# Kernel tuning notes

Measured on AMD Instinct MI355X. Metric: run time of the kernel, lower is better.

Reference implementation:

```python
import jax, jax.numpy as jnp
import numpy as np
import math

B, C, HLAT, WLON = 1, 256, 46, 90
HEADS = 8
KC = 256   # k_channels (defaults to in_channels)
OC = 256   # out_channels (defaults to in_channels)


def _cc_weights(n):
    # Clenshaw-Curtis quadrature weights on n nodes x_k = cos(k*pi/(n-1)) over [-1, 1]
    # (torch-harmonics 'equiangular' grid quadrature); weights sum to 2.
    N = n - 1
    k = np.arange(n)
    j = np.arange(1, N // 2 + 1)
    b = np.where(2 * j == N, 1.0, 2.0)
    s = (b / (4.0 * j**2 - 1.0))[None, :] * np.cos(2.0 * np.pi * np.outer(k, j) / N)
    w = (1.0 - s.sum(axis=1)) * (2.0 / N)
    w[0] *= 0.5
    w[-1] *= 0.5
    return w


def _log_quad_weights(nlat, nlon):
    wgl = _cc_weights(nlat).astype(np.float32)            # [nlat]
    qw = 2.0 * np.pi * wgl / nlon                          # [nlat]
    qw = np.tile(qw.reshape(-1, 1), (1, nlon)).flatten()   # [nlat*nlon]
    return np.log(qw).reshape(1, 1, -1)                    # (1, 1, N)


def setup_inputs() -> dict:
    key = jax.random.key(0)
    ks = jax.random.split(key, 6)
    scale_qkv = math.sqrt(3.0 / C)
    scale_proj = math.sqrt(3.0 / OC)
    uni = lambda k, shp, s: s * (2.0 * jax.random.uniform(k, shp, dtype=jnp.float32) - 1.0)
    return {
        "query": jax.random.normal(ks[0], (B, C, HLAT, WLON), dtype=jnp.float32),
        "q_w": uni(ks[1], (KC, C), scale_qkv),
        "q_b": jnp.zeros((KC,), dtype=jnp.float32),
        "k_w": uni(ks[2], (KC, C), scale_qkv),
        "k_b": jnp.zeros((KC,), dtype=jnp.float32),
        "v_w": uni(ks[3], (OC, C), scale_qkv),
        "v_b": jnp.zeros((OC,), dtype=jnp.float32),
        "p_w": uni(ks[4], (OC, OC), scale_proj),
        "p_b": jnp.zeros((OC,), dtype=jnp.float32),
        "log_qw": jnp.asarray(_log_quad_weights(HLAT, WLON)),
    }


def _conv1x1(x, w, b):
    # 1x1 conv == per-pixel channel GEMM
    return jnp.einsum("bchw,kc->bkhw", x, w) + b[None, :, None, None]


def _to_seq(x, heads):
    # [B, heads*d, H, W] -> [B, heads, H*W, d]
    b, c, h, w = x.shape
    d = c // heads
    return x.reshape(b, heads, d, h, w).transpose(0, 1, 3, 4, 2).reshape(b, heads, h * w, d)


def reference(query, q_w, q_b, k_w, k_b, v_w, v_b, p_w, p_b, log_qw):
    # key = value = query (self-attention path of the module)
    q = _conv1x1(query, q_w, q_b)
    k = _conv1x1(query, k_w, k_b)
    v = _conv1x1(query, v_w, v_b)

    qs = _to_seq(q, HEADS)   # [B, h, N, dk]
    ks = _to_seq(k, HEADS)   # [B, h, M, dk]
    vs = _to_seq(v, HEADS)   # [B, h, M, dv]

    dk = KC // HEADS
    scale = 1.0 / math.sqrt(dk)  # SDPA default scale
    # scores with additive log-quadrature-weight bias over keys
    scores = jnp.einsum("bhnd,bhmd->bhnm", qs, ks) * scale + log_qw[:, :, None, :]
    attn = jax.nn.softmax(scores, axis=-1)
    out = jnp.einsum("bhnm,bhmd->bhnd", attn, vs)  # [B, h, N, dv]

    bb, hh, nn, dv = out.shape
    out = out.transpose(0, 1, 3, 2).reshape(bb, hh * dv, HLAT, WLON)
    out = _conv1x1(out, p_w, p_b)
    return out
```

## Files before the change

kernel.cpp:

```cpp
#include <hip/hip_runtime.h>

#define N_SEQ 4140
#define NP    4160
#define C_IN  256
#define HEADS 8
#define NT32  130
#define HN    (HEADS * N_SEQ)
#define LOG2E 1.4426950408889634f
#define SCALE2 (0.17677669529663687f * LOG2E)

typedef _Float16 f16x8 __attribute__((ext_vector_type(8)));
typedef _Float16 f16x2 __attribute__((ext_vector_type(2)));
typedef float    f32x16 __attribute__((ext_vector_type(16)));

__device__ inline unsigned short f16b(float x) {
    union { _Float16 h; unsigned short s; } c;
    c.h = (_Float16)x;
    return c.s;
}
__device__ inline f16x2 pkrtz(float a, float b) {
    auto r = __builtin_amdgcn_cvt_pkrtz(a, b);
    union { decltype(r) i; f16x2 o; } c;
    c.i = r;
    return c.o;
}
__device__ inline void permswap(unsigned &a, unsigned &b) {
    asm volatile("v_permlane32_swap_b32 %0, %1" : "+v"(a), "+v"(b));
}

__global__ __launch_bounds__(256) void prep_kernel(
    const float* __restrict__ x, const float* __restrict__ log_qw,
    const float* __restrict__ q_w, const float* __restrict__ k_w,
    const float* __restrict__ v_w, const float* __restrict__ p_w,
    unsigned short* __restrict__ xt, float* __restrict__ lw2,
    unsigned short* __restrict__ wf, unsigned short* __restrict__ pwf)
{
    if (blockIdx.x < NT32) {
        __shared__ unsigned short tile[32][33];
        const int tx = threadIdx.x & 31, ty = threadIdx.x >> 5;
        const int n0 = blockIdx.x * 32, c0 = blockIdx.y * 32;
#pragma unroll
        for (int i = 0; i < 4; ++i) {
            const int c = c0 + ty * 4 + i;
            const int n = n0 + tx;
            const float v = (n < N_SEQ) ? x[(size_t)c * N_SEQ + n] : 0.f;
            tile[tx][ty * 4 + i] = f16b(v);
        }
        __syncthreads();
#pragma unroll
        for (int i = 0; i < 4; ++i) {
            const int nl = ty * 4 + i;
            xt[(size_t)(n0 + nl) * C_IN + c0 + tx] = tile[nl][tx];
        }
    } else {
        const int bid = (blockIdx.x - NT32) * 8 + blockIdx.y;
        for (int i = bid * 256 + threadIdx.x; i < 262144 + NP; i += 24 * 256) {
            if (i < 65536)        wf[i] = f16b(q_w[i] * SCALE2);
            else if (i < 131072)  wf[i] = f16b(k_w[i - 65536]);
            else if (i < 196608)  wf[i] = f16b(v_w[i - 131072]);
            else if (i < 262144)  pwf[i - 196608] = f16b(p_w[i - 196608]);
            else {
                const int j = i - 262144;
                lw2[j] = (j < N_SEQ) ? log_qw[j] * LOG2E : -1e30f;
            }
        }
    }
}

__global__ __launch_bounds__(64) void qkv_mfma(
    const unsigned short* __restrict__ xt, const unsigned short* __restrict__ wf,
    const float* __restrict__ q_b, const float* __restrict__ k_b,
    const float* __restrict__ v_b,
    unsigned short* __restrict__ qo, unsigned short* __restrict__ ko,
    unsigned short* __restrict__ vo)
{
    const int lane = threadIdx.x;
    const int col = lane & 31, hi = lane >> 5;
    const int bid = blockIdx.x;
    const int ot = bid / NT32, nt = bid % NT32;
    const int n0 = nt * 32;

    if (ot < 16) {
        const unsigned short* arow = xt + (size_t)(n0 + col) * C_IN + hi * 8;
        const unsigned short* brow = wf + (size_t)(ot * 32 + col) * C_IN + hi * 8;
        const float bias = (ot < 8) ? q_b[ot * 32 + col] * SCALE2
                                    : k_b[(ot - 8) * 32 + col];
        f32x16 acc0, acc1;
#pragma unroll
        for (int r = 0; r < 16; ++r) { acc0[r] = bias; acc1[r] = 0.f; }
#pragma unroll
        for (int t = 0; t < 8; ++t) {
            const f16x8 af0 = *(const f16x8*)(const void*)(arow + t * 16);
            const f16x8 bf0 = *(const f16x8*)(const void*)(brow + t * 16);
            const f16x8 af1 = *(const f16x8*)(const void*)(arow + (t + 8) * 16);
            const f16x8 bf1 = *(const f16x8*)(const void*)(brow + (t + 8) * 16);
            acc0 = __builtin_amdgcn_mfma_f32_32x32x16_f16(af0, bf0, acc0, 0, 0, 0);
            acc1 = __builtin_amdgcn_mfma_f32_32x32x16_f16(af1, bf1, acc1, 0, 0, 0);
        }
        unsigned short* dst = (ot < 8) ? qo : ko;
        const int h = ot & 7;
#pragma unroll
        for (int r = 0; r < 16; ++r) {
            const int rl = (r & 3) + 8 * (r >> 2) + 4 * hi;
            dst[(size_t)(h * NP + n0 + rl) * 32 + col] = f16b(acc0[r] + acc1[r]);
        }
    } else {
        const int h = ot - 16;
        const unsigned short* arow = wf + (size_t)(512 + h * 32 + col) * C_IN + hi * 8;
        const unsigned short* brow = xt + (size_t)(n0 + col) * C_IN + hi * 8;
        const float* vb4 = v_b + h * 32 + 4 * hi;
        const float4 c0 = *(const float4*)(vb4);
        const float4 c1 = *(const float4*)(vb4 + 8);
        const float4 c2 = *(const float4*)(vb4 + 16);
        const float4 c3 = *(const float4*)(vb4 + 24);
        f32x16 acc0, acc1;
        acc0[0]=c0.x; acc0[1]=c0.y; acc0[2]=c0.z; acc0[3]=c0.w;
        acc0[4]=c1.x; acc0[5]=c1.y; acc0[6]=c1.z; acc0[7]=c1.w;
        acc0[8]=c2.x; acc0[9]=c2.y; acc0[10]=c2.z; acc0[11]=c2.w;
        acc0[12]=c3.x; acc0[13]=c3.y; acc0[14]=c3.z; acc0[15]=c3.w;
#pragma unroll
        for (int r = 0; r < 16; ++r) acc1[r] = 0.f;
#pragma unroll
        for (int t = 0; t < 8; ++t) {
            const f16x8 af0 = *(const f16x8*)(const void*)(arow + t * 16);
            const f16x8 bf0 = *(const f16x8*)(const void*)(brow + t * 16);
            const f16x8 af1 = *(const f16x8*)(const void*)(arow + (t + 8) * 16);
            const f16x8 bf1 = *(const f16x8*)(const void*)(brow + (t + 8) * 16);
            acc0 = __builtin_amdgcn_mfma_f32_32x32x16_f16(af0, bf0, acc0, 0, 0, 0);
            acc1 = __builtin_amdgcn_mfma_f32_32x32x16_f16(af1, bf1, acc1, 0, 0, 0);
        }
#pragma unroll
        for (int r = 0; r < 16; ++r) {
            const int d = (r & 3) + 8 * (r >> 2) + 4 * hi;
            vo[((size_t)(h * NT32 + nt) * 32 + d) * 32 + col] = f16b(acc0[r] + acc1[r]);
        }
    }
}

__global__ __launch_bounds__(64) void attn_mfma_kernel(
    const unsigned short* __restrict__ qb, const unsigned short* __restrict__ kb,
    const unsigned short* __restrict__ vb, const float* __restrict__ lw2,
    float* __restrict__ pm, float* __restrict__ pl, float* __restrict__ pacc,
    int tiles_per_z)
{
    const int lane = threadIdx.x;
    const int col = lane & 31;
    const int hi = lane >> 5;
    const int job = blockIdx.x;
    const int h = job / 65;
    const int pt = job % 65;
    const int z = blockIdx.y;

    const int qrowA = pt * 64 + col;
    const int qrowB = qrowA + 32;
    const unsigned short* qpA = qb + ((size_t)(h * NP + qrowA)) * 32 + hi * 8;
    const unsigned short* qpB = qb + ((size_t)(h * NP + qrowB)) * 32 + hi * 8;
    const f16x8 qfA0 = *(const f16x8*)(const void*)(qpA);
    const f16x8 qfA1 = *(const f16x8*)(const void*)(qpA + 16);
    const f16x8 qfB0 = *(const f16x8*)(const void*)(qpB);
    const f16x8 qfB1 = *(const f16x8*)(const void*)(qpB + 16);

    f32x16 oA, oB;
#pragma unroll
    for (int r = 0; r < 16; ++r) { oA[r] = 0.f; oB[r] = 0.f; }
    float mA = -1e30f, lsA = 0.f;
    float mB = -1e30f, lsB = 0.f;
    const f16x2 one2 = { (_Float16)1.f, (_Float16)1.f };

    const int t0 = z * tiles_per_z;
    const int t1 = min(NT32, t0 + tiles_per_z);
    const unsigned short* kbase = kb + (size_t)h * NP * 32;
    const unsigned short* vbase = vb + (size_t)h * NT32 * 1024;

    for (int t = t0; t < t1; ++t) {
        const int k0 = t * 32;
        const unsigned short* kp = kbase + (size_t)(k0 + col) * 32 + hi * 8;
        const f16x8 ka0 = *(const f16x8*)(const void*)(kp);
        const f16x8 ka1 = *(const f16x8*)(const void*)(kp + 16);
        const unsigned short* vp = vbase + (size_t)t * 1024 + col * 32 + hi * 8;
        const f16x8 va0 = *(const f16x8*)(const void*)(vp);
        const f16x8 va1 = *(const f16x8*)(const void*)(vp + 16);

        const float* lw4 = lw2 + k0 + 4 * hi;
        const float4 w0 = *(const float4*)(lw4);
        const float4 w1 = *(const float4*)(lw4 + 8);
        const float4 w2 = *(const float4*)(lw4 + 16);
        const float4 w3 = *(const float4*)(lw4 + 24);
        f32x16 sA;
        sA[0]=w0.x; sA[1]=w0.y; sA[2]=w0.z; sA[3]=w0.w;
        sA[4]=w1.x; sA[5]=w1.y; sA[6]=w1.z; sA[7]=w1.w;
        sA[8]=w2.x; sA[9]=w2.y; sA[10]=w2.z; sA[11]=w2.w;
        sA[12]=w3.x; sA[13]=w3.y; sA[14]=w3.z; sA[15]=w3.w;
        f32x16 sB = sA;

        sA = __builtin_amdgcn_mfma_f32_32x32x16_f16(ka0, qfA0, sA, 0, 0, 0);
        sB = __builtin_amdgcn_mfma_f32_32x32x16_f16(ka0, qfB0, sB, 0, 0, 0);
        sA = __builtin_amdgcn_mfma_f32_32x32x16_f16(ka1, qfA1, sA, 0, 0, 0);
        sB = __builtin_amdgcn_mfma_f32_32x32x16_f16(ka1, qfB1, sB, 0, 0, 0);

        const float a0m = fmaxf(fmaxf(sA[0], sA[1]), sA[2]);
        const float a1m = fmaxf(fmaxf(sA[3], sA[4]), sA[5]);
        const float a2m = fmaxf(fmaxf(sA[6], sA[7]), sA[8]);
        const float a3m = fmaxf(fmaxf(sA[9], sA[10]), sA[11]);
        const float a4m = fmaxf(fmaxf(sA[12], sA[13]), sA[14]);
        const float cmaxA = fmaxf(fmaxf(fmaxf(a0m, a1m), a2m),
                                  fmaxf(fmaxf(a3m, a4m), sA[15]));
        const float b0m = fmaxf(fmaxf(sB[0], sB[1]), sB[2]);
        const float b1m = fmaxf(fmaxf(sB[3], sB[4]), sB[5]);
        const float b2m = fmaxf(fmaxf(sB[6], sB[7]), sB[8]);
        const float b3m = fmaxf(fmaxf(sB[9], sB[10]), sB[11]);
        const float b4m = fmaxf(fmaxf(sB[12], sB[13]), sB[14]);
        const float cmaxB = fmaxf(fmaxf(fmaxf(b0m, b1m), b2m),
                                  fmaxf(fmaxf(b3m, b4m), sB[15]));

        if (!__all(cmaxA - mA <= 8.0f)) {
            float cw = fmaxf(cmaxA, __shfl_xor(cmaxA, 32));
            const float mnew = fmaxf(mA, cw);
            const float esc = __builtin_amdgcn_exp2f(mA - mnew);
            lsA *= esc;
#pragma unroll
            for (int r = 0; r < 16; ++r) oA[r] *= esc;
            mA = mnew;
        }
        if (!__all(cmaxB - mB <= 8.0f)) {
            float cw = fmaxf(cmaxB, __shfl_xor(cmaxB, 32));
            const float mnew = fmaxf(mB, cw);
            const float esc = __builtin_amdgcn_exp2f(mB - mnew);
            lsB *= esc;
#pragma unroll
            for (int r = 0; r < 16; ++r) oB[r] *= esc;
            mB = mnew;
        }

        float pA[16], pB[16];
#pragma unroll
        for (int r = 0; r < 16; ++r) {
            pA[r] = __builtin_amdgcn_exp2f(sA[r] - mA);
            pB[r] = __builtin_amdgcn_exp2f(sB[r] - mB);
        }

        union PK { f16x2 h[4]; unsigned u[4]; f16x8 v; };
        {
            PK k0p, k1p;
            k0p.h[0] = pkrtz(pA[0], pA[1]);
            k0p.h[1] = pkrtz(pA[2], pA[3]);
            k0p.h[2] = pkrtz(pA[4], pA[5]);
            k0p.h[3] = pkrtz(pA[6], pA[7]);
            k1p.h[0] = pkrtz(pA[8], pA[9]);
            k1p.h[1] = pkrtz(pA[10], pA[11]);
            k1p.h[2] = pkrtz(pA[12], pA[13]);
            k1p.h[3] = pkrtz(pA[14], pA[15]);
            float sa = __builtin_amdgcn_fdot2(k0p.h[0], one2, 0.f, false);
            float sb = __builtin_amdgcn_fdot2(k0p.h[1], one2, 0.f, false);
            sa = __builtin_amdgcn_fdot2(k0p.h[2], one2, sa, false);
            sb = __builtin_amdgcn_fdot2(k0p.h[3], one2, sb, false);
            sa = __builtin_amdgcn_fdot2(k1p.h[0], one2, sa, false);
            sb = __builtin_amdgcn_fdot2(k1p.h[1], one2, sb, false);
            sa = __builtin_amdgcn_fdot2(k1p.h[2], one2, sa, false);
            sb = __builtin_amdgcn_fdot2(k1p.h[3], one2, sb, false);
            lsA += sa + sb;
            permswap(k0p.u[0], k0p.u[2]);
            permswap(k0p.u[1], k0p.u[3]);
            oA = __builtin_amdgcn_mfma_f32_32x32x16_f16(va0, k0p.v, oA, 0, 0, 0);
            permswap(k1p.u[0], k1p.u[2]);
            permswap(k1p.u[1], k1p.u[3]);
            oA = __builtin_amdgcn_mfma_f32_32x32x16_f16(va1, k1p.v, oA, 0, 0, 0);
        }
        {
            PK k0p, k1p;
            k0p.h[0] = pkrtz(pB[0], pB[1]);
            k0p.h[1] = pkrtz(pB[2], pB[3]);
            k0p.h[2] = pkrtz(pB[4], pB[5]);
            k0p.h[3] = pkrtz(pB[6], pB[7]);
            k1p.h[0] = pkrtz(pB[8], pB[9]);
            k1p.h[1] = pkrtz(pB[10], pB[11]);
            k1p.h[2] = pkrtz(pB[12], pB[13]);
            k1p.h[3] = pkrtz(pB[14], pB[15]);
            float sa = __builtin_amdgcn_fdot2(k0p.h[0], one2, 0.f, false);
            float sb = __builtin_amdgcn_fdot2(k0p.h[1], one2, 0.f, false);
            sa = __builtin_amdgcn_fdot2(k0p.h[2], one2, sa, false);
            sb = __builtin_amdgcn_fdot2(k0p.h[3], one2, sb, false);
            sa = __builtin_amdgcn_fdot2(k1p.h[0], one2, sa, false);
            sb = __builtin_amdgcn_fdot2(k1p.h[1], one2, sb, false);
            sa = __builtin_amdgcn_fdot2(k1p.h[2], one2, sa, false);
            sb = __builtin_amdgcn_fdot2(k1p.h[3], one2, sb, false);
            lsB += sa + sb;
            permswap(k0p.u[0], k0p.u[2]);
            permswap(k0p.u[1], k0p.u[3]);
            oB = __builtin_amdgcn_mfma_f32_32x32x16_f16(va0, k0p.v, oB, 0, 0, 0);
            permswap(k1p.u[0], k1p.u[2]);
            permswap(k1p.u[1], k1p.u[3]);
            oB = __builtin_amdgcn_mfma_f32_32x32x16_f16(va1, k1p.v, oB, 0, 0, 0);
        }
    }

    lsA += __shfl_xor(lsA, 32);
    lsB += __shfl_xor(lsB, 32);

    if (qrowA < N_SEQ) {
        const size_t qi = (size_t)h * N_SEQ + qrowA;
        if (hi == 0) {
            pm[(size_t)z * HN + qi] = mA;
            pl[(size_t)z * HN + qi] = lsA;
        }
        float* pa = pacc + ((size_t)z * HN + qi) * 32;
#pragma unroll
        for (int r = 0; r < 16; ++r)
            pa[(r & 3) + 8 * (r >> 2) + 4 * hi] = oA[r];
    }
    if (qrowB < N_SEQ) {
        const size_t qi = (size_t)h * N_SEQ + qrowB;
        if (hi == 0) {
            pm[(size_t)z * HN + qi] = mB;
            pl[(size_t)z * HN + qi] = lsB;
        }
        float* pa = pacc + ((size_t)z * HN + qi) * 32;
#pragma unroll
        for (int r = 0; r < 16; ++r)
            pa[(r & 3) + 8 * (r >> 2) + 4 * hi] = oB[r];
    }
}

__global__ __launch_bounds__(256) void merge_kernel(
    const float* __restrict__ pm, const float* __restrict__ pl,
    const float* __restrict__ pacc, unsigned short* __restrict__ at_t, int nz)
{
    const int gid = blockIdx.x * 256 + threadIdx.x;
    if (gid >= HN * 4) return;
    const int idx = gid >> 2;
    const int sub = gid & 3;
    const int h = idx / N_SEQ;
    const int n = idx - h * N_SEQ;

    float mg = pm[idx];
    for (int zz = 1; zz < nz; ++zz) mg = fmaxf(mg, pm[(size_t)zz * HN + idx]);

    float lg = 0.f;
    float acc[8];
#pragma unroll
    for (int d = 0; d < 8; ++d) acc[d] = 0.f;
    for (int zz = 0; zz < nz; ++zz) {
        const float e = exp2f(pm[(size_t)zz * HN + idx] - mg);
        lg += pl[(size_t)zz * HN + idx] * e;
        const float* pa = pacc + ((size_t)zz * HN + idx) * 32 + sub * 8;
#pragma unroll
        for (int d = 0; d < 8; ++d) acc[d] = fmaf(pa[d], e, acc[d]);
    }
    const float inv = 1.0f / lg;
    union { unsigned short s[8]; uint4 u; } ph;
#pragma unroll
    for (int d = 0; d < 8; ++d) ph.s[d] = f16b(acc[d] * inv);
    *(uint4*)(at_t + (size_t)n * C_IN + h * 32 + sub * 8) = ph.u;
}

__global__ __launch_bounds__(64) void proj_mfma(
    const unsigned short* __restrict__ at_t, const unsigned short* __restrict__ pwf,
    const float* __restrict__ p_b, float* __restrict__ out)
{
    const int lane = threadIdx.x;
    const int col = lane & 31, hi = lane >> 5;
    const int tile = blockIdx.x;
    const int ot = tile / NT32, nt = tile % NT32;
    const int n0 = nt * 32;

    const unsigned short* arow = pwf + (size_t)(ot * 32 + col) * C_IN + hi * 8;
    const unsigned short* brow = at_t + (size_t)(n0 + col) * C_IN + hi * 8;

    const float* pb4 = p_b + ot * 32 + 4 * hi;
    const float4 c0 = *(const float4*)(pb4);
    const float4 c1 = *(const float4*)(pb4 + 8);
    const float4 c2 = *(const float4*)(pb4 + 16);
    const float4 c3 = *(const float4*)(pb4 + 24);
    f32x16 acca, accb;
    acca[0]=c0.x; acca[1]=c0.y; acca[2]=c0.z; acca[3]=c0.w;
    acca[4]=c1.x; acca[5]=c1.y; acca[6]=c1.z; acca[7]=c1.w;
    acca[8]=c2.x; acca[9]=c2.y; acca[10]=c2.z; acca[11]=c2.w;
    acca[12]=c3.x; acca[13]=c3.y; acca[14]=c3.z; acca[15]=c3.w;
#pragma unroll
    for (int r = 0; r < 16; ++r) accb[r] = 0.f;

#pragma unroll
    for (int t = 0; t < 8; ++t) {
        const f16x8 afa = *(const f16x8*)(const void*)(arow + t * 16);
        const f16x8 bfa = *(const f16x8*)(const void*)(brow + t * 16);
        const f16x8 afb = *(const f16x8*)(const void*)(arow + (t + 8) * 16);
        const f16x8 bfb = *(const f16x8*)(const void*)(brow + (t + 8) * 16);
        acca = __builtin_amdgcn_mfma_f32_32x32x16_f16(afa, bfa, acca, 0, 0, 0);
        accb = __builtin_amdgcn_mfma_f32_32x32x16_f16(afb, bfb, accb, 0, 0, 0);
    }

    const int n = n0 + col;
    if (n < N_SEQ) {
#pragma unroll
        for (int r = 0; r < 16; ++r) {
            const int oc = ot * 32 + (r & 3) + 8 * (r >> 2) + 4 * hi;
            out[(size_t)oc * N_SEQ + n] = acca[r] + accb[r];
        }
    }
}

extern "C" void kernel_launch(void* const* d_in, const int* in_sizes, int n_in,
                              void* d_out, int out_size, void* d_ws, size_t ws_size,
                              hipStream_t stream) {
    const float* query  = (const float*)d_in[0];
    const float* q_w    = (const float*)d_in[1];
    const float* q_b    = (const float*)d_in[2];
    const float* k_w    = (const float*)d_in[3];
    const float* k_b    = (const float*)d_in[4];
    const float* v_w    = (const float*)d_in[5];
    const float* v_b    = (const float*)d_in[6];
    const float* p_w    = (const float*)d_in[7];
    const float* p_b    = (const float*)d_in[8];
    const float* log_qw = (const float*)d_in[9];

    const size_t HNP32 = (size_t)HEADS * NP * 32;

    unsigned short* xt  = (unsigned short*)d_ws;
    unsigned short* qb  = xt + (size_t)NP * C_IN;
    unsigned short* kb  = qb + HNP32;
    unsigned short* vb  = kb + HNP32;
    unsigned short* wf  = vb + HNP32;
    unsigned short* pwf = wf + 768 * 256;
    float* lw2 = (float*)(pwf + 256 * 256);
    float* pm  = lw2 + NP;
    unsigned short* at_t = qb;

    const size_t base_bytes = (size_t)((char*)pm - (char*)d_ws);
    const size_t per_z = (size_t)HN * 34 * sizeof(float);
    int nz = 1;
    if      (ws_size >= base_bytes + 8 * per_z) nz = 8;
    else if (ws_size >= base_bytes + 4 * per_z) nz = 4;
    else if (ws_size >= base_bytes + 2 * per_z) nz = 2;
    const int tiles_per_z = (NT32 + nz - 1) / nz;

    float* pl   = pm + (size_t)nz * HN;
    float* pacc = pl + (size_t)nz * HN;

    prep_kernel<<<dim3(NT32 + 3, 8), 256, 0, stream>>>(
        query, log_qw, q_w, k_w, v_w, p_w, xt, lw2, wf, pwf);

    qkv_mfma<<<dim3(3120), 64, 0, stream>>>(
        xt, wf, q_b, k_b, v_b, qb, kb, vb);

    attn_mfma_kernel<<<dim3(520, nz), 64, 0, stream>>>(
        qb, kb, vb, lw2, pm, pl, pacc, tiles_per_z);

    merge_kernel<<<dim3((HN * 4 + 255) / 256), 256, 0, stream>>>(
        pm, pl, pacc, at_t, nz);

    proj_mfma<<<dim3(1040), 64, 0, stream>>>(
        at_t, pwf, p_b, (float*)d_out);
}
```

Baseline: 164.0 us.

## Use one 32-row query tile per wave and store normalized fp16 partials

The attention kernel now processes a single 32-row query tile per wavefront instead of two, doubling the grid and asking for higher occupancy through launch bounds. Each wave normalizes its partial output by its own sum and stores it as fp16, halving the bytes written and later read by the merge kernel. The merge weights partials by exp(m)*l to stay consistent with the normalization. The cost is that K/V tiles are loaded twice as often per query and partial outputs carry fp16 rounding.

```diff
diff --git a/kernel.cpp b/kernel.cpp
--- a/kernel.cpp
+++ b/kernel.cpp
@@ -21,6 +21,12 @@
 __device__ inline f16x2 pkrtz(float a, float b) {
     auto r = __builtin_amdgcn_cvt_pkrtz(a, b);
     union { decltype(r) i; f16x2 o; } c;
+    c.i = r;
+    return c.o;
+}
+__device__ inline unsigned pkrtz_u(float a, float b) {
+    auto r = __builtin_amdgcn_cvt_pkrtz(a, b);
+    union { decltype(r) i; unsigned o; } c;
     c.i = r;
     return c.o;
 }
@@ -137,34 +143,29 @@
     }
 }
 
-__global__ __launch_bounds__(64) void attn_mfma_kernel(
+__global__ __launch_bounds__(64, 8) void attn_mfma_kernel(
     const unsigned short* __restrict__ qb, const unsigned short* __restrict__ kb,
     const unsigned short* __restrict__ vb, const float* __restrict__ lw2,
-    float* __restrict__ pm, float* __restrict__ pl, float* __restrict__ pacc,
-    int tiles_per_z)
+    float* __restrict__ pm, float* __restrict__ pl,
+    unsigned short* __restrict__ pacc, int tiles_per_z)
 {
     const int lane = threadIdx.x;
     const int col = lane & 31;
     const int hi = lane >> 5;
     const int job = blockIdx.x;
-    const int h = job / 65;
-    const int pt = job % 65;
+    const int h = job / NT32;
+    const int qt = job % NT32;
     const int z = blockIdx.y;
 
-    const int qrowA = pt * 64 + col;
-    const int qrowB = qrowA + 32;
-    const unsigned short* qpA = qb + ((size_t)(h * NP + qrowA)) * 32 + hi * 8;
-    const unsigned short* qpB = qb + ((size_t)(h * NP + qrowB)) * 32 + hi * 8;
-    const f16x8 qfA0 = *(const f16x8*)(const void*)(qpA);
-    const f16x8 qfA1 = *(const f16x8*)(const void*)(qpA + 16);
-    const f16x8 qfB0 = *(const f16x8*)(const void*)(qpB);
-    const f16x8 qfB1 = *(const f16x8*)(const void*)(qpB + 16);
-
-    f32x16 oA, oB;
-#pragma unroll
-    for (int r = 0; r < 16; ++r) { oA[r] = 0.f; oB[r] = 0.f; }
-    float mA = -1e30f, lsA = 0.f;
-    float mB = -1e30f, lsB = 0.f;
+    const int qrow = qt * 32 + col;
+    const unsigned short* qp = qb + ((size_t)(h * NP + qrow)) * 32 + hi * 8;
+    const f16x8 qf0 = *(const f16x8*)(const void*)(qp);
+    const f16x8 qf1 = *(const f16x8*)(const void*)(qp + 16);
+
+    f32x16 o;
+#pragma unroll
+    for (int r = 0; r < 16; ++r) o[r] = 0.f;
+    float m = -1e30f, lsum = 0.f;
     const f16x2 one2 = { (_Float16)1.f, (_Float16)1.f };
 
     const int t0 = z * tiles_per_z;
@@ -186,144 +187,89 @@
         const float4 w1 = *(const float4*)(lw4 + 8);
         const float4 w2 = *(const float4*)(lw4 + 16);
         const float4 w3 = *(const float4*)(lw4 + 24);
-        f32x16 sA;
-        sA[0]=w0.x; sA[1]=w0.y; sA[2]=w0.z; sA[3]=w0.w;
-        sA[4]=w1.x; sA[5]=w1.y; sA[6]=w1.z; sA[7]=w1.w;
-        sA[8]=w2.x; sA[9]=w2.y; sA[10]=w2.z; sA[11]=w2.w;
-        sA[12]=w3.x; sA[13]=w3.y; sA[14]=w3.z; sA[15]=w3.w;
-        f32x16 sB = sA;
-
-        sA = __builtin_amdgcn_mfma_f32_32x32x16_f16(ka0, qfA0, sA, 0, 0, 0);
-        sB = __builtin_amdgcn_mfma_f32_32x32x16_f16(ka0, qfB0, sB, 0, 0, 0);
-        sA = __builtin_amdgcn_mfma_f32_32x32x16_f16(ka1, qfA1, sA, 0, 0, 0);
-        sB = __builtin_amdgcn_mfma_f32_32x32x16_f16(ka1, qfB1, sB, 0, 0, 0);
-
-        const float a0m = fmaxf(fmaxf(sA[0], sA[1]), sA[2]);
-        const float a1m = fmaxf(fmaxf(sA[3], sA[4]), sA[5]);
-        const float a2m = fmaxf(fmaxf(sA[6], sA[7]), sA[8]);
-        const float a3m = fmaxf(fmaxf(sA[9], sA[10]), sA[11]);
-        const float a4m = fmaxf(fmaxf(sA[12], sA[13]), sA[14]);
-        const float cmaxA = fmaxf(fmaxf(fmaxf(a0m, a1m), a2m),
-                                  fmaxf(fmaxf(a3m, a4m), sA[15]));
-        const float b0m = fmaxf(fmaxf(sB[0], sB[1]), sB[2]);
-        const float b1m = fmaxf(fmaxf(sB[3], sB[4]), sB[5]);
-        const float b2m = fmaxf(fmaxf(sB[6], sB[7]), sB[8]);
-        const float b3m = fmaxf(fmaxf(sB[9], sB[10]), sB[11]);
-        const float b4m = fmaxf(fmaxf(sB[12], sB[13]), sB[14]);
-        const float cmaxB = fmaxf(fmaxf(fmaxf(b0m, b1m), b2m),
-                                  fmaxf(fmaxf(b3m, b4m), sB[15]));
-
-        if (!__all(cmaxA - mA <= 8.0f)) {
-            float cw = fmaxf(cmaxA, __shfl_xor(cmaxA, 32));
-            const float mnew = fmaxf(mA, cw);
-            const float esc = __builtin_amdgcn_exp2f(mA - mnew);
-            lsA *= esc;
-#pragma unroll
-            for (int r = 0; r < 16; ++r) oA[r] *= esc;
-            mA = mnew;
-        }
-        if (!__all(cmaxB - mB <= 8.0f)) {
-            float cw = fmaxf(cmaxB, __shfl_xor(cmaxB, 32));
-            const float mnew = fmaxf(mB, cw);
-            const float esc = __builtin_amdgcn_exp2f(mB - mnew);
-            lsB *= esc;
-#pragma unroll
-            for (int r = 0; r < 16; ++r) oB[r] *= esc;
-            mB = mnew;
-        }
-
-        float pA[16], pB[16];
-#pragma unroll
-        for (int r = 0; r < 16; ++r) {
-            pA[r] = __builtin_amdgcn_exp2f(sA[r] - mA);
-            pB[r] = __builtin_amdgcn_exp2f(sB[r] - mB);
-        }
+        f32x16 s;
+        s[0]=w0.x; s[1]=w0.y; s[2]=w0.z; s[3]=w0.w;
+        s[4]=w1.x; s[5]=w1.y; s[6]=w1.z; s[7]=w1.w;
+        s[8]=w2.x; s[9]=w2.y; s[10]=w2.z; s[11]=w2.w;
+        s[12]=w3.x; s[13]=w3.y; s[14]=w3.z; s[15]=w3.w;
+
+        s = __builtin_amdgcn_mfma_f32_32x32x16_f16(ka0, qf0, s, 0, 0, 0);
+        s = __builtin_amdgcn_mfma_f32_32x32x16_f16(ka1, qf1, s, 0, 0, 0);
+
+        const float x0 = fmaxf(fmaxf(s[0], s[1]), s[2]);
+        const float x1 = fmaxf(fmaxf(s[3], s[4]), s[5]);
+        const float x2 = fmaxf(fmaxf(s[6], s[7]), s[8]);
+        const float x3 = fmaxf(fmaxf(s[9], s[10]), s[11]);
+        const float x4 = fmaxf(fmaxf(s[12], s[13]), s[14]);
+        const float cmax = fmaxf(fmaxf(fmaxf(x0, x1), x2),
+                                 fmaxf(fmaxf(x3, x4), s[15]));
+
+        if (!__all(cmax - m <= 8.0f)) {
+            float cw = fmaxf(cmax, __shfl_xor(cmax, 32));
+            const float mnew = fmaxf(m, cw);
+            const float esc = __builtin_amdgcn_exp2f(m - mnew);
+            lsum *= esc;
+#pragma unroll
+            for (int r = 0; r < 16; ++r) o[r] *= esc;
+            m = mnew;
+        }
+
+        float p[16];
+#pragma unroll
+        for (int r = 0; r < 16; ++r) p[r] = __builtin_amdgcn_exp2f(s[r] - m);
 
         union PK { f16x2 h[4]; unsigned u[4]; f16x8 v; };
-        {
-            PK k0p, k1p;
-            k0p.h[0] = pkrtz(pA[0], pA[1]);
-            k0p.h[1] = pkrtz(pA[2], pA[3]);
-            k0p.h[2] = pkrtz(pA[4], pA[5]);
-            k0p.h[3] = pkrtz(pA[6], pA[7]);
-            k1p.h[0] = pkrtz(pA[8], pA[9]);
-            k1p.h[1] = pkrtz(pA[10], pA[11]);
-            k1p.h[2] = pkrtz(pA[12], pA[13]);
-            k1p.h[3] = pkrtz(pA[14], pA[15]);
-            float sa = __builtin_amdgcn_fdot2(k0p.h[0], one2, 0.f, false);
-            float sb = __builtin_amdgcn_fdot2(k0p.h[1], one2, 0.f, false);
-            sa = __builtin_amdgcn_fdot2(k0p.h[2], one2, sa, false);
-            sb = __builtin_amdgcn_fdot2(k0p.h[3], one2, sb, false);
-            sa = __builtin_amdgcn_fdot2(k1p.h[0], one2, sa, false);
-            sb = __builtin_amdgcn_fdot2(k1p.h[1], one2, sb, false);
-            sa = __builtin_amdgcn_fdot2(k1p.h[2], one2, sa, false);
-            sb = __builtin_amdgcn_fdot2(k1p.h[3], one2, sb, false);
-            lsA += sa + sb;
-            permswap(k0p.u[0], k0p.u[2]);
-            permswap(k0p.u[1], k0p.u[3]);
-            oA = __builtin_amdgcn_mfma_f32_32x32x16_f16(va0, k0p.v, oA, 0, 0, 0);
-            permswap(k1p.u[0], k1p.u[2]);
-            permswap(k1p.u[1], k1p.u[3]);
-            oA = __builtin_amdgcn_mfma_f32_32x32x16_f16(va1, k1p.v, oA, 0, 0, 0);
-        }
-        {
-            PK k0p, k1p;
-            k0p.h[0] = pkrtz(pB[0], pB[1]);
-            k0p.h[1] = pkrtz(pB[2], pB[3]);
-            k0p.h[2] = pkrtz(pB[4], pB[5]);
-            k0p.h[3] = pkrtz(pB[6], pB[7]);
-            k1p.h[0] = pkrtz(pB[8], pB[9]);
-            k1p.h[1] = pkrtz(pB[10], pB[11]);
-            k1p.h[2] = pkrtz(pB[12], pB[13]);
-            k1p.h[3] = pkrtz(pB[14], pB[15]);
-            float sa = __builtin_amdgcn_fdot2(k0p.h[0], one2, 0.f, false);
-            float sb = __builtin_amdgcn_fdot2(k0p.h[1], one2, 0.f, false);
-            sa = __builtin_amdgcn_fdot2(k0p.h[2], one2, sa, false);
-            sb = __builtin_amdgcn_fdot2(k0p.h[3], one2, sb, false);
-            sa = __builtin_amdgcn_fdot2(k1p.h[0], one2, sa, false);
-            sb = __builtin_amdgcn_fdot2(k1p.h[1], one2, sb, false);
-            sa = __builtin_amdgcn_fdot2(k1p.h[2], one2, sa, false);
-            sb = __builtin_amdgcn_fdot2(k1p.h[3], one2, sb, false);
-            lsB += sa + sb;
-            permswap(k0p.u[0], k0p.u[2]);
-            permswap(k0p.u[1], k0p.u[3]);
-            oB = __builtin_amdgcn_mfma_f32_32x32x16_f16(va0, k0p.v, oB, 0, 0, 0);
-            permswap(k1p.u[0], k1p.u[2]);
-            permswap(k1p.u[1], k1p.u[3]);
-            oB = __builtin_amdgcn_mfma_f32_32x32x16_f16(va1, k1p.v, oB, 0, 0, 0);
-        }
-    }
-
-    lsA += __shfl_xor(lsA, 32);
-    lsB += __shfl_xor(lsB, 32);
-
-    if (qrowA < N_SEQ) {
-        const size_t qi = (size_t)h * N_SEQ + qrowA;
+        PK k0p, k1p;
+        k0p.h[0] = pkrtz(p[0], p[1]);
+        k0p.h[1] = pkrtz(p[2], p[3]);
+        k0p.h[2] = pkrtz(p[4], p[5]);
+        k0p.h[3] = pkrtz(p[6], p[7]);
+        k1p.h[0] = pkrtz(p[8], p[9]);
+        k1p.h[1] = pkrtz(p[10], p[11]);
+        k1p.h[2] = pkrtz(p[12], p[13]);
+        k1p.h[3] = pkrtz(p[14], p[15]);
+        float sa = __builtin_amdgcn_fdot2(k0p.h[0], one2, 0.f, false);
+        float sb = __builtin_amdgcn_fdot2(k0p.h[1], one2, 0.f, false);
+        sa = __builtin_amdgcn_fdot2(k0p.h[2], one2, sa, false);
+        sb = __builtin_amdgcn_fdot2(k0p.h[3], one2, sb, false);
+        sa = __builtin_amdgcn_fdot2(k1p.h[0], one2, sa, false);
+        sb = __builtin_amdgcn_fdot2(k1p.h[1], one2, sb, false);
+        sa = __builtin_amdgcn_fdot2(k1p.h[2], one2, sa, false);
+        sb = __builtin_amdgcn_fdot2(k1p.h[3], one2, sb, false);
+        lsum += sa + sb;
+        permswap(k0p.u[0], k0p.u[2]);
+        permswap(k0p.u[1], k0p.u[3]);
+        o = __builtin_amdgcn_mfma_f32_32x32x16_f16(va0, k0p.v, o, 0, 0, 0);
+        permswap(k1p.u[0], k1p.u[2]);
+        permswap(k1p.u[1], k1p.u[3]);
+        o = __builtin_amdgcn_mfma_f32_32x32x16_f16(va1, k1p.v, o, 0, 0, 0);
+    }
+
+    lsum += __shfl_xor(lsum, 32);
+
+    if (qrow < N_SEQ) {
+        const size_t qi = (size_t)h * N_SEQ + qrow;
         if (hi == 0) {
-            pm[(size_t)z * HN + qi] = mA;
-            pl[(size_t)z * HN + qi] = lsA;
-        }
-        float* pa = pacc + ((size_t)z * HN + qi) * 32;
-#pragma unroll
-        for (int r = 0; r < 16; ++r)
-            pa[(r & 3) + 8 * (r >> 2) + 4 * hi] = oA[r];
-    }
-    if (qrowB < N_SEQ) {
-        const size_t qi = (size_t)h * N_SEQ + qrowB;
-        if (hi == 0) {
-            pm[(size_t)z * HN + qi] = mB;
-            pl[(size_t)z * HN + qi] = lsB;
-        }
-        float* pa = pacc + ((size_t)z * HN + qi) * 32;
-#pragma unroll
-        for (int r = 0; r < 16; ++r)
-            pa[(r & 3) + 8 * (r >> 2) + 4 * hi] = oB[r];
+            pm[(size_t)z * HN + qi] = m;
+            pl[(size_t)z * HN + qi] = lsum;
+        }
+        const float inv = 1.0f / lsum;
+        unsigned short* pa = pacc + ((size_t)z * HN + qi) * 32;
+#pragma unroll
+        for (int g = 0; g < 4; ++g) {
+            const int d0 = g * 8 + 4 * hi;
+            uint2 w;
+            w.x = pkrtz_u(o[g * 4 + 0] * inv, o[g * 4 + 1] * inv);
+            w.y = pkrtz_u(o[g * 4 + 2] * inv, o[g * 4 + 3] * inv);
+            *(uint2*)(pa + d0) = w;
+        }
     }
 }
 
 __global__ __launch_bounds__(256) void merge_kernel(
     const float* __restrict__ pm, const float* __restrict__ pl,
-    const float* __restrict__ pacc, unsigned short* __restrict__ at_t, int nz)
+    const unsigned short* __restrict__ pacc, unsigned short* __restrict__ at_t,
+    int nz)
 {
     const int gid = blockIdx.x * 256 + threadIdx.x;
     if (gid >= HN * 4) return;
@@ -340,11 +286,14 @@
 #pragma unroll
     for (int d = 0; d < 8; ++d) acc[d] = 0.f;
     for (int zz = 0; zz < nz; ++zz) {
-        const float e = exp2f(pm[(size_t)zz * HN + idx] - mg);
-        lg += pl[(size_t)zz * HN + idx] * e;
-        const float* pa = pacc + ((size_t)zz * HN + idx) * 32 + sub * 8;
-#pragma unroll
-        for (int d = 0; d < 8; ++d) acc[d] = fmaf(pa[d], e, acc[d]);
+        const float w = exp2f(pm[(size_t)zz * HN + idx] - mg)
+                      * pl[(size_t)zz * HN + idx];
+        lg += w;
+        const unsigned short* pa = pacc + ((size_t)zz * HN + idx) * 32 + sub * 8;
+        union { uint4 u; _Float16 hh[8]; } ld;
+        ld.u = *(const uint4*)pa;
+#pragma unroll
+        for (int d = 0; d < 8; ++d) acc[d] = fmaf(w, (float)ld.hh[d], acc[d]);
     }
     const float inv = 1.0f / lg;
     union { unsigned short s[8]; uint4 u; } ph;
@@ -426,15 +375,15 @@
     unsigned short* at_t = qb;
 
     const size_t base_bytes = (size_t)((char*)pm - (char*)d_ws);
-    const size_t per_z = (size_t)HN * 34 * sizeof(float);
+    const size_t per_z = (size_t)HN * 72;
     int nz = 1;
     if      (ws_size >= base_bytes + 8 * per_z) nz = 8;
     else if (ws_size >= base_bytes + 4 * per_z) nz = 4;
     else if (ws_size >= base_bytes + 2 * per_z) nz = 2;
     const int tiles_per_z = (NT32 + nz - 1) / nz;
 
-    float* pl   = pm + (size_t)nz * HN;
-    float* pacc = pl + (size_t)nz * HN;
+    float* pl = pm + (size_t)nz * HN;
+    unsigned short* pacc = (unsigned short*)(pl + (size_t)nz * HN);
 
     prep_kernel<<<dim3(NT32 + 3, 8), 256, 0, stream>>>(
         query, log_qw, q_w, k_w, v_w, p_w, xt, lw2, wf, pwf);
@@ -442,7 +391,7 @@
     qkv_mfma<<<dim3(3120), 64, 0, stream>>>(
         xt, wf, q_b, k_b, v_b, qb, kb, vb);
 
-    attn_mfma_kernel<<<dim3(520, nz), 64, 0, stream>>>(
+    attn_mfma_kernel<<<dim3(1040, nz), 64, 0, stream>>>(
         qb, kb, vb, lw2, pm, pl, pacc, tiles_per_z);
 
     merge_kernel<<<dim3((HN * 4 + 255) / 256), 256, 0, stream>>>(
```

Result: slower. 189.6 us (+15.6%).
